# Kernel optimization log

Measured on AMD Instinct MI355X. Metric: run time of the kernel, lower is better.

Reference implementation:

```python
import jax, jax.numpy as jnp
import numpy as np


def setup_inputs() -> dict:
    key = jax.random.key(0)
    k1, k2 = jax.random.split(key)
    N, z_dim, H, W = 16, 64, 32, 32
    n_latents, M, dim = 4, 1024, 16
    z = jax.random.normal(k1, (N, z_dim, H, W), dtype=jnp.float32)
    e = jax.random.normal(k2, (n_latents, M, dim), dtype=jnp.float32)
    log_sigma = jnp.zeros((1,), dtype=jnp.float32)  # init_log_sigma = 0.0
    return {"z": z, "e": e, "log_sigma": log_sigma}


def reference(z, e, log_sigma):
    N, z_dim, H, W = z.shape
    n_latents, M, dim = e.shape
    # (N, z_dim, H, W) -> (n_latents, N*H*W, dim_per_latent)
    zr = z.reshape(N, n_latents, dim, H, W)
    zr = jnp.transpose(zr, (1, 0, 3, 4, 2)).reshape(n_latents, N * H * W, dim)
    # squared euclidean distance via expansion: ||z||^2 + ||e||^2 - 2 z.e
    z_sq = jnp.sum(zr * zr, axis=-1)            # (L, P)
    e_sq = jnp.sum(e * e, axis=-1)              # (L, M)
    cross = jnp.einsum('lpd,lmd->lpm', zr, e)   # (L, P, M)
    d2 = z_sq[:, :, None] + e_sq[:, None, :] - 2.0 * cross  # (L, P, M)
    alpha = -1.0 / (2.0 * jnp.exp(log_sigma) ** 2)          # (1,)
    lse = jax.nn.logsumexp(alpha * d2, axis=1)              # reduce over points -> (L, M)
    loss = -jnp.mean(lse, axis=1)                            # (L,)
    # 0.5*z_dim*(2*log_sigma - log(e)) + log(N*H*W); log(e) == 1
    loss = loss + 0.5 * z_dim * (2.0 * log_sigma - 1.0) + jnp.float32(np.log(N * H * W))
    return jnp.mean(loss)
```

## Files before the change

### kernel.cpp

```cpp
#include <hip/hip_runtime.h>
#include <math.h>

#define NL 4
#define MM 1024
#define DD 16
#define PP 16384
#define PLANE 1024
#define NSTRIDE 65536
#define CHUNK 512
#define NCHUNK (PP / CHUNK)
#define MGROUP 128
#define NMG (MM / MGROUP)
#define ZSTR 20

#define EXP2_SCALE 8388608.0f
#define EXP2_BIAS  126.9647f

typedef _Float16 half4v  __attribute__((ext_vector_type(4)));
typedef _Float16 half8v  __attribute__((ext_vector_type(8)));
typedef float    float16v __attribute__((ext_vector_type(16)));

__global__ __launch_bounds__(256, 4)
void latent_dist_kernel(const float* __restrict__ z, const float* __restrict__ e,
                        const float* __restrict__ log_sigma, float* __restrict__ S)
{
    const int t    = threadIdx.x;
    const int lane = t & 63;
    const int wave = t >> 6;
    const int ln31 = lane & 31;
    const int hf   = lane >> 5;

    const int bid = blockIdx.x;
    const int c   = bid & (NCHUNK - 1);
    const int mg  = (bid >> 5) & (NMG - 1);
    const int l   = bid >> 8;

    const float ls    = log_sigma[0];
    const float alpha = -0.5f * __expf(-2.0f * ls);
    const float a2    = alpha * 1.44269504088896340736f;
    const float m2a2  = -2.0f * a2;

    __shared__ __attribute__((aligned(16))) _Float16 zh[CHUNK * ZSTR];
    __shared__ float azqs[CHUNK];
    __shared__ float esqs[MGROUP];

    const int n  = c >> 1;
    const int q0 = (c & 1) * CHUNK;
    const float* zb = z + (size_t)n * NSTRIDE + (size_t)l * DD * PLANE + q0;

    float sq[2] = {0.f, 0.f};
#pragma unroll
    for (int dp = 0; dp < 8; ++dp) {
#pragma unroll
        for (int j = 0; j < 2; ++j) {
            const int pl = j * 256 + t;
            float v0 = zb[(2 * dp)     * PLANE + pl];
            float v1 = zb[(2 * dp + 1) * PLANE + pl];
            sq[j] += v0 * v0 + v1 * v1;
            union { _Float16 h[2]; unsigned u; } pk;
            pk.h[0] = (_Float16)v0; pk.h[1] = (_Float16)v1;
            *(unsigned*)(&zh[pl * ZSTR + 2 * dp]) = pk.u;
        }
    }
    azqs[t]       = (sq[0] * a2 + EXP2_BIAS) * EXP2_SCALE;
    azqs[256 + t] = (sq[1] * a2 + EXP2_BIAS) * EXP2_SCALE;

    const int m0 = mg * MGROUP + wave * 32;
    const float* eb = e + ((size_t)l * MM + m0 + ln31) * DD + hf * 8;
    float4 a0 = *(const float4*)eb;
    float4 a1 = *(const float4*)(eb + 4);
    float esq_p = a0.x*a0.x + a0.y*a0.y + a0.z*a0.z + a0.w*a0.w
                + a1.x*a1.x + a1.y*a1.y + a1.z*a1.z + a1.w*a1.w;
    esq_p += __shfl_xor(esq_p, 32, 64);
    esqs[wave * 32 + ln31] = esq_p;

    half8v Af;
    Af[0] = (_Float16)(a0.x * m2a2); Af[1] = (_Float16)(a0.y * m2a2);
    Af[2] = (_Float16)(a0.z * m2a2); Af[3] = (_Float16)(a0.w * m2a2);
    Af[4] = (_Float16)(a1.x * m2a2); Af[5] = (_Float16)(a1.y * m2a2);
    Af[6] = (_Float16)(a1.z * m2a2); Af[7] = (_Float16)(a1.w * m2a2);

    __syncthreads();

    float16v biasC;
#pragma unroll
    for (int r = 0; r < 16; ++r) {
        const int row = (r & 3) + 8 * (r >> 2) + 4 * hf;
        biasC[r] = esqs[wave * 32 + row] * a2;
    }

    float16v acc;
#pragma unroll
    for (int r = 0; r < 16; ++r) acc[r] = 0.f;

    const _Float16* zrow = zh + ln31 * ZSTR + hf * 8;
#pragma unroll 2
    for (int pt = 0; pt < CHUNK / 32; ++pt) {
        const float az = azqs[pt * 32 + ln31];
        const _Float16* bp = zrow + pt * 32 * ZSTR;
        half4v b0 = *(const half4v*)bp;
        half4v b1 = *(const half4v*)(bp + 4);
        half8v Bf = __builtin_shufflevector(b0, b1, 0, 1, 2, 3, 4, 5, 6, 7);
        float16v dd = __builtin_amdgcn_mfma_f32_32x32x16_f16(Af, Bf, biasC, 0, 0, 0);
#pragma unroll
        for (int r = 0; r < 16; ++r) {
            float u = fmaf(dd[r], EXP2_SCALE, az);
            acc[r] += __uint_as_float(__float2uint_rz(u));
        }
    }

#pragma unroll
    for (int r = 0; r < 16; ++r) {
        float v = acc[r];
        v += __shfl_xor(v, 16, 64);
        v += __shfl_xor(v, 8, 64);
        v += __shfl_xor(v, 4, 64);
        v += __shfl_xor(v, 2, 64);
        v += __shfl_xor(v, 1, 64);
        acc[r] = v;
    }

    if (ln31 == 0) {
        float* Sp = S + l * MM + m0;
#pragma unroll
        for (int r = 0; r < 16; ++r) {
            const int row = (r & 3) + 8 * (r >> 2) + 4 * hf;
            atomicAdd(&Sp[row], acc[r]);
        }
    }
}

__global__ void latent_reduce_kernel(const float* __restrict__ S,
                                     const float* __restrict__ log_sigma,
                                     float* __restrict__ out)
{
    const int t = threadIdx.x;
    float s = 0.f;
#pragma unroll
    for (int k = 0; k < 4; ++k) s += __logf(S[k * 1024 + t]);
#pragma unroll
    for (int off = 32; off > 0; off >>= 1) s += __shfl_down(s, off, 64);
    __shared__ float red[16];
    if ((t & 63) == 0) red[t >> 6] = s;
    __syncthreads();
    if (t == 0) {
        float tot = 0.f;
#pragma unroll
        for (int i = 0; i < 16; ++i) tot += red[i];
        const float ls = log_sigma[0];
        out[0] = -tot / (float)(NL * MM)
               + 32.0f * (2.0f * ls - 1.0f)
               + 9.70406052783923f;
    }
}

extern "C" void kernel_launch(void* const* d_in, const int* in_sizes, int n_in,
                              void* d_out, int out_size, void* d_ws, size_t ws_size,
                              hipStream_t stream)
{
    const float* z  = (const float*)d_in[0];
    const float* e  = (const float*)d_in[1];
    const float* ls = (const float*)d_in[2];
    float* out = (float*)d_out;
    float* S   = (float*)d_ws;

    hipMemsetAsync(S, 0, NL * MM * sizeof(float), stream);
    latent_dist_kernel<<<NL * NMG * NCHUNK, 256, 0, stream>>>(z, e, ls, S);
    latent_reduce_kernel<<<1, 1024, 0, stream>>>(S, ls, out);
}
```

Baseline: 75.50 us.

## Halve point chunk and replace shuffle reduction with LDS transpose-reduce

Halves the points per block to 256, which doubles the grid so more blocks are in flight and each thread loads a single point. The per-wave cross-lane shuffle reduction over 16 accumulators is replaced by writing the accumulators to padded LDS scratch, which reuses the z buffer after a barrier. Each lane then sums one row, and one atomic per lane is issued instead of 16 atomics from a single lane. This cuts the shuffle instruction count and serialized atomics, but doubles the total number of global atomics and adds a block barrier.

```diff
diff --git a/kernel.cpp b/kernel.cpp
--- a/kernel.cpp
+++ b/kernel.cpp
@@ -7,11 +7,13 @@
 #define PP 16384
 #define PLANE 1024
 #define NSTRIDE 65536
-#define CHUNK 512
+#define CHUNK 256
 #define NCHUNK (PP / CHUNK)
 #define MGROUP 128
 #define NMG (MM / MGROUP)
 #define ZSTR 20
+#define SCR_STRIDE 33
+#define SCR_WAVE 1056
 
 #define EXP2_SCALE 8388608.0f
 #define EXP2_BIAS  126.9647f
@@ -32,38 +34,35 @@
 
     const int bid = blockIdx.x;
     const int c   = bid & (NCHUNK - 1);
-    const int mg  = (bid >> 5) & (NMG - 1);
-    const int l   = bid >> 8;
+    const int mg  = (bid >> 6) & (NMG - 1);
+    const int l   = bid >> 9;
 
     const float ls    = log_sigma[0];
     const float alpha = -0.5f * __expf(-2.0f * ls);
     const float a2    = alpha * 1.44269504088896340736f;
     const float m2a2  = -2.0f * a2;
 
-    __shared__ __attribute__((aligned(16))) _Float16 zh[CHUNK * ZSTR];
+    __shared__ __attribute__((aligned(16))) char smem[4 * SCR_WAVE * 4];
+    _Float16* zh = (_Float16*)smem;
+    float*    scr = (float*)smem;
     __shared__ float azqs[CHUNK];
     __shared__ float esqs[MGROUP];
 
-    const int n  = c >> 1;
-    const int q0 = (c & 1) * CHUNK;
+    const int n  = c >> 2;
+    const int q0 = (c & 3) * CHUNK;
     const float* zb = z + (size_t)n * NSTRIDE + (size_t)l * DD * PLANE + q0;
 
-    float sq[2] = {0.f, 0.f};
+    float sq = 0.f;
 #pragma unroll
     for (int dp = 0; dp < 8; ++dp) {
-#pragma unroll
-        for (int j = 0; j < 2; ++j) {
-            const int pl = j * 256 + t;
-            float v0 = zb[(2 * dp)     * PLANE + pl];
-            float v1 = zb[(2 * dp + 1) * PLANE + pl];
-            sq[j] += v0 * v0 + v1 * v1;
-            union { _Float16 h[2]; unsigned u; } pk;
-            pk.h[0] = (_Float16)v0; pk.h[1] = (_Float16)v1;
-            *(unsigned*)(&zh[pl * ZSTR + 2 * dp]) = pk.u;
-        }
+        float v0 = zb[(2 * dp)     * PLANE + t];
+        float v1 = zb[(2 * dp + 1) * PLANE + t];
+        sq += v0 * v0 + v1 * v1;
+        union { _Float16 h[2]; unsigned u; } pk;
+        pk.h[0] = (_Float16)v0; pk.h[1] = (_Float16)v1;
+        *(unsigned*)(&zh[t * ZSTR + 2 * dp]) = pk.u;
     }
-    azqs[t]       = (sq[0] * a2 + EXP2_BIAS) * EXP2_SCALE;
-    azqs[256 + t] = (sq[1] * a2 + EXP2_BIAS) * EXP2_SCALE;
+    azqs[t] = (sq * a2 + EXP2_BIAS) * EXP2_SCALE;
 
     const int m0 = mg * MGROUP + wave * 32;
     const float* eb = e + ((size_t)l * MM + m0 + ln31) * DD + hf * 8;
@@ -109,25 +108,20 @@
         }
     }
 
+    __syncthreads();
+    float* scrw = scr + wave * SCR_WAVE;
 #pragma unroll
     for (int r = 0; r < 16; ++r) {
-        float v = acc[r];
-        v += __shfl_xor(v, 16, 64);
-        v += __shfl_xor(v, 8, 64);
-        v += __shfl_xor(v, 4, 64);
-        v += __shfl_xor(v, 2, 64);
-        v += __shfl_xor(v, 1, 64);
-        acc[r] = v;
+        const int row = (r & 3) + 8 * (r >> 2) + 4 * hf;
+        scrw[row * SCR_STRIDE + ln31] = acc[r];
     }
-
-    if (ln31 == 0) {
-        float* Sp = S + l * MM + m0;
+    const float* rp = scrw + ln31 * SCR_STRIDE + hf * 16;
+    float s = 0.f;
 #pragma unroll
-        for (int r = 0; r < 16; ++r) {
-            const int row = (r & 3) + 8 * (r >> 2) + 4 * hf;
-            atomicAdd(&Sp[row], acc[r]);
-        }
-    }
+    for (int j = 0; j < 16; ++j) s += rp[j];
+    s += __shfl_xor(s, 32, 64);
+    if (hf == 0)
+        atomicAdd(&S[l * MM + m0 + ln31], s);
 }
 
 __global__ void latent_reduce_kernel(const float* __restrict__ S,
```

New measurement: 69.29 us. 8.2% less time.
